# Kernel optimization log

Hardware: AMD Instinct MI355X
Metric: run time of the kernel (lower is better)

The kernel has to match this reference:

```python
import jax, jax.numpy as jnp
import numpy as np

H, W, C = 512, 512, 288  # SAT resolution and channels (ntheta*nphi = 9*32)
N = 131072               # number of query points


def setup_inputs() -> dict:
    key = jax.random.key(0)
    k1, k2 = jax.random.split(key)
    sat = jax.random.normal(k1, (H, W, C), dtype=jnp.float32)
    x = jax.random.uniform(k2, (N, 4), dtype=jnp.float32)  # [cu, cv, du, dv] in [0,1)
    return {"sat": sat, "x": x, "start_idx": -1, "len_idx": 1}


def reference(sat, x, start_idx, len_idx):
    Hh, Ww, Cc = sat.shape
    resf = jnp.array([Hh, Ww], jnp.float32)
    resi = jnp.array([Hh, Ww], jnp.int32)
    duv = jnp.array([1.0 / Hh, 1.0 / Ww], jnp.float32)
    sat_flat = sat.reshape(-1, Cc)
    if start_idx >= 0:
        sat_flat = sat_flat[:, start_idx:start_idx + len_idx]

    def sample(u):  # u: [N, 2] -> [N, Cq]
        idx = jnp.floor(u * resf - 0.5).astype(jnp.int32)
        bad = jnp.any((idx < 0) | (idx >= resi), axis=-1, keepdims=True)
        lin = jnp.clip(idx[:, 0], 0, Hh - 1) * Ww + jnp.clip(idx[:, 1], 0, Ww - 1)
        return jnp.where(bad, 0.0, sat_flat[lin])

    def query(suv, euv):  # inclusive box sum via 4-corner SAT lookup
        r = sample(euv) + sample(suv - duv)
        r = r - sample(jnp.stack([suv[:, 0] - duv[0], euv[:, 1]], -1))
        r = r - sample(jnp.stack([euv[:, 0], suv[:, 1] - duv[1]], -1))
        return r

    cuv = x[:, :2]
    d = x[:, 2:]
    suv = cuv - d / 2
    euv = cuv + d / 2
    # per-axis swap when the footprint extent is negative
    nsuv = jnp.where(d < 0, euv, suv)
    neuv = jnp.where(d < 0, suv, euv)
    # toroidal wraparound into [0, 1)
    nsuv = nsuv - jnp.floor(nsuv)
    neuv = neuv - jnp.floor(neuv)
    sx, sy = nsuv[:, 0], nsuv[:, 1]
    ex, ey = neuv[:, 0], neuv[:, 1]
    n = x.shape[0]
    bru = jnp.full((n,), 1.0 - duv[0] / 2, jnp.float32)
    brv = jnp.full((n,), 1.0 - duv[1] / 2, jnp.float32)
    tlu = 1.0 - bru
    tlv = 1.0 - brv
    st = lambda a, b: jnp.stack([a, b], -1)

    # case 1: no wrap on either axis
    c = ((sx <= ex) & (sy <= ey))[:, None]
    result = jnp.where(c, query(nsuv, neuv), 0.0)
    # case 2: wrap in u only -> two boxes
    c = ((sx > ex) & (sy <= ey))[:, None]
    result += jnp.where(c, query(nsuv, st(bru, ey)), 0.0)
    result += jnp.where(c, query(st(tlu, sy), neuv), 0.0)
    # case 3: wrap in v only -> two boxes
    c = ((sx <= ex) & (sy > ey))[:, None]
    result += jnp.where(c, query(nsuv, st(ex, brv)), 0.0)
    result += jnp.where(c, query(st(sx, tlv), neuv), 0.0)
    # case 4: wrap in both -> four boxes
    c = ((sx > ex) & (sy > ey))[:, None]
    result += jnp.where(c, query(st(tlu, tlv), neuv), 0.0)
    result += jnp.where(c, query(nsuv, st(bru, brv)), 0.0)
    result += jnp.where(c, query(st(sx, tlv), st(bru, ey)), 0.0)
    result += jnp.where(c, query(st(tlu, sy), st(ex, brv)), 0.0)
    return result
```

## Files before the change

### kernel.cpp

```cpp
#include <hip/hip_runtime.h>


constexpr int Hdim = 512;
constexpr int Wdim = 512;
constexpr int Cdim = 288;

typedef float f32x4 __attribute__((ext_vector_type(4)));

__device__ __forceinline__ void prep(float u0, float u1, float s,
                                     int& off, float& sgn) {
    int i0 = (int)floorf(u0 * 512.0f - 0.5f);
    int i1 = (int)floorf(u1 * 512.0f - 0.5f);
    bool ok = ((unsigned)i0 < (unsigned)Hdim) && ((unsigned)i1 < (unsigned)Wdim);
    off = ok ? (i0 * Wdim + i1) * Cdim : 0;
    sgn = ok ? s : 0.0f;
}

__device__ __forceinline__ void prep_query(float su, float sv, float eu, float ev,
                                           int* off, float* sgn) {
    const float du = 1.0f / (float)Hdim;
    const float dv = 1.0f / (float)Wdim;
    prep(eu, ev, 1.0f, off[0], sgn[0]);
    prep(su - du, sv - dv, 1.0f, off[1], sgn[1]);
    prep(su - du, ev, -1.0f, off[2], sgn[2]);
    prep(eu, sv - dv, -1.0f, off[3], sgn[3]);
}

template <int K>
__device__ __forceinline__ void gather(const float* __restrict__ sat,
                                       const int* off, const float* sgn,
                                       int lane, int widx, float tmask,
                                       f32x4& a, f32x4& b) {
    f32x4 v[K], w[K];
#pragma unroll
    for (int k = 0; k < K; ++k) {
        const f32x4* __restrict__ row = (const f32x4*)(sat + off[k]);
        v[k] = row[lane];
        w[k] = row[widx];
    }
#pragma unroll
    for (int k = 0; k < K; ++k) {
        float s = sgn[k];
        float t = s * tmask;
        a += s * v[k];
        b += t * w[k];
    }
}

__global__ __launch_bounds__(256) void sat_query_kernel(
    const float* __restrict__ sat, const float* __restrict__ x,
    float* __restrict__ out, int n) {
    int wave = (int)((blockIdx.x * blockDim.x + threadIdx.x) >> 6);
    int lane = (int)(threadIdx.x & 63);
    if (wave >= n) return;

    float4 xr = ((const float4*)x)[wave];
    float cu = xr.x, cv = xr.y, d0 = xr.z, d1 = xr.w;

    const float du = 1.0f / (float)Hdim;
    const float dv = 1.0f / (float)Wdim;

    float su = cu - d0 * 0.5f, eu = cu + d0 * 0.5f;
    float sv = cv - d1 * 0.5f, ev = cv + d1 * 0.5f;
    float nsu = (d0 < 0.0f) ? eu : su, neu = (d0 < 0.0f) ? su : eu;
    float nsv = (d1 < 0.0f) ? ev : sv, nev = (d1 < 0.0f) ? sv : ev;
    nsu -= floorf(nsu); neu -= floorf(neu);
    nsv -= floorf(nsv); nev -= floorf(nev);

    float sx = nsu, sy = nsv, ex = neu, ey = nev;
    float bru = 1.0f - du * 0.5f, brv = 1.0f - dv * 0.5f;
    float tlu = du * 0.5f, tlv = dv * 0.5f;

    f32x4 acc_a = {0.f, 0.f, 0.f, 0.f};
    f32x4 acc_b = {0.f, 0.f, 0.f, 0.f};

    int widx = (lane & 7) + 64;
    float tmask = (lane < 8) ? 1.0f : 0.0f;

    bool wx = (sx > ex), wy = (sy > ey);
    int off[8];
    float sgn[8];
    if (!wx && !wy) {
        prep_query(sx, sy, ex, ey, off, sgn);
        gather<4>(sat, off, sgn, lane, widx, tmask, acc_a, acc_b);
    } else if (wx && !wy) {
        prep_query(sx, sy, bru, ey, off, sgn);
        prep_query(tlu, sy, ex, ey, off + 4, sgn + 4);
        gather<8>(sat, off, sgn, lane, widx, tmask, acc_a, acc_b);
    } else if (!wx && wy) {
        prep_query(sx, sy, ex, brv, off, sgn);
        prep_query(sx, tlv, ex, ey, off + 4, sgn + 4);
        gather<8>(sat, off, sgn, lane, widx, tmask, acc_a, acc_b);
    } else {
        prep_query(tlu, tlv, ex, ey, off, sgn);
        prep_query(sx, sy, bru, brv, off + 4, sgn + 4);
        gather<8>(sat, off, sgn, lane, widx, tmask, acc_a, acc_b);
        prep_query(sx, tlv, bru, ey, off, sgn);
        prep_query(tlu, sy, ex, brv, off + 4, sgn + 4);
        gather<8>(sat, off, sgn, lane, widx, tmask, acc_a, acc_b);
    }

    f32x4* __restrict__ orow = (f32x4*)(out + (size_t)wave * Cdim);
    __builtin_nontemporal_store(acc_a, orow + lane);
    if (lane < 8) __builtin_nontemporal_store(acc_b, orow + lane + 64);
}

extern "C" void kernel_launch(void* const* d_in, const int* in_sizes, int n_in,
                              void* d_out, int out_size, void* d_ws, size_t ws_size,
                              hipStream_t stream) {
    const float* sat = (const float*)d_in[0];
    const float* x   = (const float*)d_in[1];
    float* out = (float*)d_out;
    int n = in_sizes[1] / 4;

    int rows_per_block = 4;
    int blocks = (n + rows_per_block - 1) / rows_per_block;
    sat_query_kernel<<<dim3(blocks), dim3(256), 0, stream>>>(sat, x, out, n);
}
```

Baseline: 475.7 us.

## Factor SAT corner lookups per axis to deduplicate wrapped-box gathers

Splits each corner lookup into independent per-axis index and sign terms, then forms the outer product of u-terms and v-terms. Wrapped boxes share corners, and some corners fall out of range, so this needs 6 gathers instead of 8 for single-axis wrap and 9 instead of 16 for double wrap. Row offsets go through readfirstlane so they stay scalar, and the per-lane tail mask multiply is dropped. Summing the terms in a different order can change floating-point rounding slightly compared with the original box-by-box accumulation.

```diff
diff --git a/kernel.cpp b/kernel.cpp
--- a/kernel.cpp
+++ b/kernel.cpp
@@ -7,44 +7,50 @@
 
 typedef float f32x4 __attribute__((ext_vector_type(4)));
 
-__device__ __forceinline__ void prep(float u0, float u1, float s,
-                                     int& off, float& sgn) {
-    int i0 = (int)floorf(u0 * 512.0f - 0.5f);
-    int i1 = (int)floorf(u1 * 512.0f - 0.5f);
-    bool ok = ((unsigned)i0 < (unsigned)Hdim) && ((unsigned)i1 < (unsigned)Wdim);
-    off = ok ? (i0 * Wdim + i1) * Cdim : 0;
+__device__ __forceinline__ void axis_prep(float u, float s, int& idx, float& sgn) {
+    int i = (int)floorf(u * 512.0f - 0.5f);
+    bool ok = (unsigned)i < 512u;
+    idx = ok ? i : 0;
     sgn = ok ? s : 0.0f;
-}
-
-__device__ __forceinline__ void prep_query(float su, float sv, float eu, float ev,
-                                           int* off, float* sgn) {
-    const float du = 1.0f / (float)Hdim;
-    const float dv = 1.0f / (float)Wdim;
-    prep(eu, ev, 1.0f, off[0], sgn[0]);
-    prep(su - du, sv - dv, 1.0f, off[1], sgn[1]);
-    prep(su - du, ev, -1.0f, off[2], sgn[2]);
-    prep(eu, sv - dv, -1.0f, off[3], sgn[3]);
 }
 
 template <int K>
 __device__ __forceinline__ void gather(const float* __restrict__ sat,
                                        const int* off, const float* sgn,
-                                       int lane, int widx, float tmask,
+                                       int lane, int widx,
                                        f32x4& a, f32x4& b) {
     f32x4 v[K], w[K];
 #pragma unroll
     for (int k = 0; k < K; ++k) {
-        const f32x4* __restrict__ row = (const f32x4*)(sat + off[k]);
+        int offk = __builtin_amdgcn_readfirstlane(off[k]);
+        const f32x4* __restrict__ row = (const f32x4*)(sat + offk);
         v[k] = row[lane];
         w[k] = row[widx];
     }
 #pragma unroll
     for (int k = 0; k < K; ++k) {
         float s = sgn[k];
-        float t = s * tmask;
         a += s * v[k];
-        b += t * w[k];
+        b += s * w[k];
     }
+}
+
+template <int NU, int NV>
+__device__ __forceinline__ void run_case(const float* __restrict__ sat,
+                                         const int* iu, const float* fu,
+                                         const int* iv, const float* fv,
+                                         int lane, int widx,
+                                         f32x4& a, f32x4& b) {
+    int off[NU * NV];
+    float sgn[NU * NV];
+#pragma unroll
+    for (int i = 0; i < NU; ++i)
+#pragma unroll
+        for (int j = 0; j < NV; ++j) {
+            off[i * NV + j] = (iu[i] * Wdim + iv[j]) * Cdim;
+            sgn[i * NV + j] = fu[i] * fv[j];
+        }
+    gather<NU * NV>(sat, off, sgn, lane, widx, a, b);
 }
 
 __global__ __launch_bounds__(256) void sat_query_kernel(
@@ -57,8 +63,7 @@
     float4 xr = ((const float4*)x)[wave];
     float cu = xr.x, cv = xr.y, d0 = xr.z, d1 = xr.w;
 
-    const float du = 1.0f / (float)Hdim;
-    const float dv = 1.0f / (float)Wdim;
+    const float du = 1.0f / 512.0f;
 
     float su = cu - d0 * 0.5f, eu = cu + d0 * 0.5f;
     float sv = cv - d1 * 0.5f, ev = cv + d1 * 0.5f;
@@ -67,37 +72,31 @@
     nsu -= floorf(nsu); neu -= floorf(neu);
     nsv -= floorf(nsv); nev -= floorf(nev);
 
-    float sx = nsu, sy = nsv, ex = neu, ey = nev;
-    float bru = 1.0f - du * 0.5f, brv = 1.0f - dv * 0.5f;
-    float tlu = du * 0.5f, tlv = dv * 0.5f;
+    bool wx = nsu > neu;
+    bool wy = nsv > nev;
+
+    int iu[3]; float fu[3];
+    axis_prep(neu,       1.0f, iu[0], fu[0]);
+    axis_prep(nsu - du, -1.0f, iu[1], fu[1]);
+    iu[2] = Hdim - 1; fu[2] = 1.0f;
+
+    int iv[3]; float fv[3];
+    axis_prep(nev,       1.0f, iv[0], fv[0]);
+    axis_prep(nsv - du, -1.0f, iv[1], fv[1]);
+    iv[2] = Wdim - 1; fv[2] = 1.0f;
 
     f32x4 acc_a = {0.f, 0.f, 0.f, 0.f};
     f32x4 acc_b = {0.f, 0.f, 0.f, 0.f};
+    int widx = (lane & 7) + 64;
 
-    int widx = (lane & 7) + 64;
-    float tmask = (lane < 8) ? 1.0f : 0.0f;
-
-    bool wx = (sx > ex), wy = (sy > ey);
-    int off[8];
-    float sgn[8];
     if (!wx && !wy) {
-        prep_query(sx, sy, ex, ey, off, sgn);
-        gather<4>(sat, off, sgn, lane, widx, tmask, acc_a, acc_b);
+        run_case<2, 2>(sat, iu, fu, iv, fv, lane, widx, acc_a, acc_b);
     } else if (wx && !wy) {
-        prep_query(sx, sy, bru, ey, off, sgn);
-        prep_query(tlu, sy, ex, ey, off + 4, sgn + 4);
-        gather<8>(sat, off, sgn, lane, widx, tmask, acc_a, acc_b);
+        run_case<3, 2>(sat, iu, fu, iv, fv, lane, widx, acc_a, acc_b);
     } else if (!wx && wy) {
-        prep_query(sx, sy, ex, brv, off, sgn);
-        prep_query(sx, tlv, ex, ey, off + 4, sgn + 4);
-        gather<8>(sat, off, sgn, lane, widx, tmask, acc_a, acc_b);
+        run_case<2, 3>(sat, iu, fu, iv, fv, lane, widx, acc_a, acc_b);
     } else {
-        prep_query(tlu, tlv, ex, ey, off, sgn);
-        prep_query(sx, sy, bru, brv, off + 4, sgn + 4);
-        gather<8>(sat, off, sgn, lane, widx, tmask, acc_a, acc_b);
-        prep_query(sx, tlv, bru, ey, off, sgn);
-        prep_query(tlu, sy, ex, brv, off + 4, sgn + 4);
-        gather<8>(sat, off, sgn, lane, widx, tmask, acc_a, acc_b);
+        run_case<3, 3>(sat, iu, fu, iv, fv, lane, widx, acc_a, acc_b);
     }
 
     f32x4* __restrict__ orow = (f32x4*)(out + (size_t)wave * Cdim);
```

Result: no change. 472.3 us (median of 2 runs) (-0.7%).
